# Kernel tuning notes

Hardware: AMD Instinct MI355X
Metric: run time of the kernel (lower is better)

## Reference

```python
import jax, jax.numpy as jnp
import numpy as np

TOP_K = 2


def setup_inputs() -> dict:
    key = jax.random.key(0)
    k0, k1, k2, k3, k4 = jax.random.split(key, 5)
    B, S, H, I, E = 4, 2048, 1024, 2816, 8
    s_h = 1.0 / np.sqrt(H)
    s_i = 1.0 / np.sqrt(I)
    return {
        "x": jax.random.normal(k0, (B, S, H), jnp.float32),
        # nn.Linear weights are stored as [out_features, in_features]
        "w_router": jax.random.normal(k1, (E, H), jnp.float32) * s_h,   # gate: H -> E
        "w_gate": jax.random.normal(k2, (E, I, H), jnp.float32) * s_h,  # per-expert gate_proj
        "w_up": jax.random.normal(k3, (E, I, H), jnp.float32) * s_h,    # per-expert up_proj
        "w_down": jax.random.normal(k4, (E, H, I), jnp.float32) * s_i,  # per-expert down_proj
    }


def reference(x, w_router, w_gate, w_up, w_down):
    B, S, H = x.shape
    E = w_router.shape[0]
    xf = x.reshape(-1, H)                      # [T, H], T = B*S

    # --- Router: softmax over experts, top-k, renormalize weights ---
    logits = jnp.einsum("th,eh->te", xf, w_router)        # [T, E]
    probs = jax.nn.softmax(logits, axis=-1)
    topw, topi = jax.lax.top_k(probs, TOP_K)              # [T, k]
    topw = topw / jnp.sum(topw, axis=-1, keepdims=True)

    # Per-token combine weight for each expert: sum_k w[t,k] * 1[idx[t,k]==e]
    onehot = (topi[..., None] == jnp.arange(E)).astype(x.dtype)  # [T, k, E]
    combine = jnp.einsum("tk,tke->te", topw, onehot)             # [T, E]

    # --- Experts: SwiGLU MLP per expert on all tokens, masked combine ---
    # (masked-dense in the original == gather-compute mathematically,
    # since silu(0)*0 = 0 and the projections have no bias)
    gate = jax.nn.silu(jnp.einsum("th,eih->eti", xf, w_gate))    # [E, T, I]
    up = jnp.einsum("th,eih->eti", xf, w_up)                     # [E, T, I]
    down = jnp.einsum("eti,ehi->eth", gate * up, w_down)         # [E, T, H]

    out = jnp.einsum("eth,te->th", down, combine)                # [T, H]
    return out.reshape(B, S, H)
```

## Files before the change

kernel.cpp:

```cpp
#include <hip/hip_runtime.h>

#define TT 8192
#define HD 1024
#define ID 2816
#define NE 8
#define NID2 (2*ID)

typedef __attribute__((ext_vector_type(8))) short short8;
typedef __attribute__((ext_vector_type(4))) float f32x4;

#define WS_TOP2I 0
#define WS_TOP2W 65536
#define WS_CNT   131072
#define WS_OFF   131136
#define WS_CUR   131200
#define WS_TMAP  131328
#define WS_SLOTW 196864
#define WS_T2S   262400
#define WS_XB    1048576ULL
#define WS_WGU   (WS_XB  + 16777216ULL)
#define WS_WDB   (WS_WGU + 92274688ULL)
#define WS_ACT   (WS_WDB + 46137344ULL)

__device__ __forceinline__ unsigned int pack_bf2(float lo, float hi) {
  unsigned int ul = __builtin_bit_cast(unsigned int, lo) + 0x8000u;
  unsigned int uh = __builtin_bit_cast(unsigned int, hi) + 0x8000u;
  return (uh & 0xffff0000u) | (ul >> 16);
}

__device__ __forceinline__ unsigned short f2bf(float f) {
  unsigned int u = __builtin_bit_cast(unsigned int, f);
  return (unsigned short)((u + 0x8000u) >> 16);
}

__device__ __forceinline__ void gload16(const void* g, void* l) {
  __builtin_amdgcn_global_load_lds(
      (const __attribute__((address_space(1))) unsigned int*)g,
      (__attribute__((address_space(3))) unsigned int*)l, 16, 0, 0);
}

__global__ __launch_bounds__(256) void router_kernel(
    const float* __restrict__ x, const float* __restrict__ wr,
    int* __restrict__ top2i, float* __restrict__ top2w,
    unsigned short* __restrict__ xb)
{
  int tid  = threadIdx.x;
  int lane = tid & 63;
  int t    = blockIdx.x * 4 + (tid >> 6);

  const float4* xp = (const float4*)(x + (size_t)t * HD + lane * 16);
  float4 xv[4];
  #pragma unroll
  for (int j = 0; j < 4; ++j) xv[j] = xp[j];

  uint4 v0, v1;
  v0.x = pack_bf2(xv[0].x, xv[0].y); v0.y = pack_bf2(xv[0].z, xv[0].w);
  v0.z = pack_bf2(xv[1].x, xv[1].y); v0.w = pack_bf2(xv[1].z, xv[1].w);
  v1.x = pack_bf2(xv[2].x, xv[2].y); v1.y = pack_bf2(xv[2].z, xv[2].w);
  v1.z = pack_bf2(xv[3].x, xv[3].y); v1.w = pack_bf2(xv[3].z, xv[3].w);
  uint4* xrow = (uint4*)(xb + (size_t)t * HD + lane * 16);
  xrow[0] = v0; xrow[1] = v1;

  float acc[NE];
  #pragma unroll
  for (int e = 0; e < NE; ++e) {
    const float4* wp = (const float4*)(wr + (size_t)e * HD + lane * 16);
    float s = 0.f;
    #pragma unroll
    for (int j = 0; j < 4; ++j) {
      float4 w = wp[j];
      s += xv[j].x * w.x + xv[j].y * w.y + xv[j].z * w.z + xv[j].w * w.w;
    }
    acc[e] = s;
  }
  #pragma unroll
  for (int d = 1; d < 64; d <<= 1) {
    #pragma unroll
    for (int e = 0; e < NE; ++e) acc[e] += __shfl_xor(acc[e], d, 64);
  }
  int   i0 = 0; float m0 = acc[0];
  #pragma unroll
  for (int e = 1; e < NE; ++e) if (acc[e] > m0) { m0 = acc[e]; i0 = e; }
  int   i1 = -1; float m1 = -3.4e38f;
  #pragma unroll
  for (int e = 0; e < NE; ++e) if (e != i0 && acc[e] > m1) { m1 = acc[e]; i1 = e; }

  float e1 = __expf(m1 - m0);
  float w0 = 1.f / (1.f + e1);
  float w1 = e1 * w0;

  if (lane == 0) {
    top2i[2 * t] = i0;  top2i[2 * t + 1] = i1;
    top2w[2 * t] = w0;  top2w[2 * t + 1] = w1;
  }
}

__global__ __launch_bounds__(256) void count_scan_kernel(
    const int* __restrict__ top2i,
    int* __restrict__ counts, int* __restrict__ offsets, int* __restrict__ cursors)
{
  __shared__ int s_cnt[NE];
  int tid = threadIdx.x;
  if (tid < NE) s_cnt[tid] = 0;
  __syncthreads();

  int c0=0,c1=0,c2=0,c3=0,c4=0,c5=0,c6=0,c7=0;
  for (int t = tid; t < TT; t += 256) {
    int e0 = top2i[2 * t], e1 = top2i[2 * t + 1];
    c0 += __popcll(__ballot(e0 == 0)) + __popcll(__ballot(e1 == 0));
    c1 += __popcll(__ballot(e0 == 1)) + __popcll(__ballot(e1 == 1));
    c2 += __popcll(__ballot(e0 == 2)) + __popcll(__ballot(e1 == 2));
    c3 += __popcll(__ballot(e0 == 3)) + __popcll(__ballot(e1 == 3));
    c4 += __popcll(__ballot(e0 == 4)) + __popcll(__ballot(e1 == 4));
    c5 += __popcll(__ballot(e0 == 5)) + __popcll(__ballot(e1 == 5));
    c6 += __popcll(__ballot(e0 == 6)) + __popcll(__ballot(e1 == 6));
    c7 += __popcll(__ballot(e0 == 7)) + __popcll(__ballot(e1 == 7));
  }
  if ((tid & 63) == 0) {
    atomicAdd(&s_cnt[0], c0); atomicAdd(&s_cnt[1], c1);
    atomicAdd(&s_cnt[2], c2); atomicAdd(&s_cnt[3], c3);
    atomicAdd(&s_cnt[4], c4); atomicAdd(&s_cnt[5], c5);
    atomicAdd(&s_cnt[6], c6); atomicAdd(&s_cnt[7], c7);
  }
  __syncthreads();
  if (tid == 0) {
    int run = 0;
    #pragma unroll
    for (int e = 0; e < NE; ++e) {
      counts[e] = s_cnt[e]; offsets[e] = run; cursors[e] = run; run += s_cnt[e];
    }
    offsets[NE] = run;
  }
}

__global__ __launch_bounds__(256) void place_kernel(
    const int* __restrict__ top2i, const float* __restrict__ top2w,
    int* __restrict__ cursors,
    int* __restrict__ token_map, float* __restrict__ slot_w, int* __restrict__ tok2slot)
{
  int tid  = threadIdx.x;
  int lane = tid & 63;
  int t    = blockIdx.x * 256 + tid;

  #pragma unroll
  for (int k = 0; k < 2; ++k) {
    int   e = top2i[2 * t + k];
    float w = top2w[2 * t + k];
    #pragma unroll
    for (int ee = 0; ee < NE; ++ee) {
      unsigned long long m = __ballot(e == ee);
      if (e == ee) {
        int leader = __ffsll((long long)m) - 1;
        int pre    = __popcll(m & ((1ull << lane) - 1ull));
        int base   = 0;
        if (lane == leader) base = atomicAdd(&cursors[ee], (int)__popcll(m));
        base = __shfl(base, leader, 64);
        token_map[base + pre] = t;
        slot_w[base + pre]    = w;
        tok2slot[2 * t + k]   = base + pre;
      }
    }
  }
}

__global__ __launch_bounds__(256) void cvt_wgu_kernel(
    const float* __restrict__ wg, const float* __restrict__ wu,
    unsigned short* __restrict__ wgu)
{
  int e   = blockIdx.y;
  int idx = blockIdx.x * 256 + threadIdx.x;
  int col8 = idx & 127;
  int rr   = idx >> 7;
  int blk  = rr >> 8;
  int win  = rr & 255;
  const float* srow = (win < 128)
      ? wg + ((size_t)e * ID + blk * 128 + win) * HD
      : wu + ((size_t)e * ID + blk * 128 + (win - 128)) * HD;
  const float4* p = (const float4*)(srow + col8 * 8);
  float4 a = p[0], b = p[1];
  uint4 v;
  v.x = pack_bf2(a.x, a.y); v.y = pack_bf2(a.z, a.w);
  v.z = pack_bf2(b.x, b.y); v.w = pack_bf2(b.z, b.w);
  *(uint4*)(wgu + ((size_t)e * NID2 + rr) * HD + col8 * 8) = v;
}

__global__ __launch_bounds__(256) void cvt_bf16_kernel(
    const float* __restrict__ in, unsigned short* __restrict__ out, int n8)
{
  int i = blockIdx.x * 256 + threadIdx.x;
  if (i >= n8) return;
  const float4* p = (const float4*)(in + (size_t)i * 8);
  float4 a = p[0], b = p[1];
  uint4 v;
  v.x = pack_bf2(a.x, a.y); v.y = pack_bf2(a.z, a.w);
  v.z = pack_bf2(b.x, b.y); v.w = pack_bf2(b.z, b.w);
  ((uint4*)out)[i] = v;
}


#define VW(N) asm volatile("s_waitcnt vmcnt(" #N ")" ::: "memory")
#define BAR() __builtin_amdgcn_s_barrier()

#define ISSUE(t) { \
    size_t k1 = (size_t)((t) * 32); \
    char* db = ldsc + (((t) & 3) * 32768u) + (unsigned)tid * 16; \
    gload16(aS[0] + k1, db);            gload16(aS[1] + k1, db + 8192); \
    gload16(bS[0] + k1, db + 16384);    gload16(bS[1] + k1, db + 24576); }

#define BODY(t) { \
    const char* sa = ldsc + (((t) & 3) * 32768u); \
    const char* sb = sa + 16384; \
    short8 af[8], bfr[4]; \
    _Pragma("unroll") for (int n = 0; n < 4; ++n) \
      bfr[n] = *(const short8*)(sb + (wc * 64 + n * 16 + arow) * 64 + kx); \
    _Pragma("unroll") for (int m = 0; m < 8; ++m) \
      af[m] = *(const short8*)(sa + (wr * 128 + m * 16 + arow) * 64 + kx); \
    __builtin_amdgcn_s_setprio(1); \
    _Pragma("unroll") for (int m = 0; m < 8; ++m) \
      _Pragma("unroll") for (int n = 0; n < 4; ++n) \
        acc[m][n] = __builtin_amdgcn_mfma_f32_16x16x32_bf16(af[m], bfr[n], acc[m][n], 0, 0, 0); \
    __builtin_amdgcn_s_setprio(0); }

#define KLOOP(NT) { \
    ISSUE(0); ISSUE(1); ISSUE(2); \
    int t = 0; \
    for (; t < (NT) - 3; ++t) { VW(8); BAR(); ISSUE(t + 3); BODY(t); } \
    VW(8); BAR(); BODY(t); ++t; \
    VW(4); BAR(); BODY(t); ++t; \
    VW(0); BAR(); BODY(t); }

#define XCD_DECODE(NX, NY) \
  int nwg  = (NX) * (NY) * NE; \
  int flat = blockIdx.x + (NX) * (blockIdx.y + (NY) * blockIdx.z); \
  int qq   = nwg >> 3; \
  int wg   = (flat & 7) * qq + (flat >> 3); \
  int bx   = wg % (NX); \
  int rem  = wg / (NX); \
  int y    = rem % (NY); \
  int e    = rem / (NY);

__global__ __launch_bounds__(512, 2) void gemm1_fast(
    const unsigned short* __restrict__ xb, const unsigned short* __restrict__ wgu,
    const int* __restrict__ counts, const int* __restrict__ offsets,
    const int* __restrict__ token_map, unsigned short* __restrict__ act)
{
  extern __shared__ char smem[];
  char* ldsc = smem;

  XCD_DECODE(8, 22)
  int cnt = counts[e];
  int off = offsets[e];

  int tid  = threadIdx.x;
  int lane = tid & 63;
  int w    = tid >> 6;
  int wr   = w >> 2;
  int wc   = w & 3;

  int srow = tid >> 2;
  int colE = (((tid & 3) ^ ((tid >> 2) & 3)) << 3);
  int arow = lane & 15;
  int kx   = (((lane >> 4) ^ (lane & 3)) << 4);
  int prow = (lane >> 4) << 2;

  for (int t0 = bx * 256; t0 < cnt; t0 += 2048) {
    const unsigned short* aS[2];
    const unsigned short* bS[2];
    #pragma unroll
    for (int j = 0; j < 2; ++j) {
      int row  = srow + 128 * j;
      int tr   = t0 + row;
      int slot = off + (tr < cnt ? tr : cnt - 1);
      aS[j] = xb  + (size_t)token_map[slot] * HD + colE;
      bS[j] = wgu + ((size_t)e * NID2 + (size_t)y * 256 + row) * HD + colE;
    }

    f32x4 zf = {0.f, 0.f, 0.f, 0.f};
    f32x4 acc[8][4];
    #pragma unroll
    for (int m = 0; m < 8; ++m)
      #pragma unroll
      for (int n = 0; n < 4; ++n) acc[m][n] = zf;

    KLOOP(HD / 32);

    __syncthreads();
    float* xch = (float*)smem;
    if (wc >= 2) {
      float* base = xch + (size_t)((wr * 2 + (wc - 2)) * 8192);
      #pragma unroll
      for (int m = 0; m < 8; ++m)
        #pragma unroll
        for (int n = 0; n < 4; ++n)
          #pragma unroll
          for (int r = 0; r < 4; ++r)
            base[(m * 16 + prow + r) * 64 + n * 16 + arow] = acc[m][n][r];
    }
    __syncthreads();
    if (wc < 2) {
      const float* base = xch + (size_t)((wr * 2 + wc) * 8192);
      int i0 = y * 128 + wc * 64;
      #pragma unroll
      for (int m = 0; m < 8; ++m) {
        #pragma unroll
        for (int r = 0; r < 4; ++r) {
          int row = wr * 128 + m * 16 + prow + r;
          int tr2 = t0 + row;
          if (tr2 >= cnt) continue;
          size_t ob = (size_t)(off + tr2) * ID + i0 + arow;
          #pragma unroll
          for (int n = 0; n < 4; ++n) {
            float g = acc[m][n][r];
            float u = base[(m * 16 + prow + r) * 64 + n * 16 + arow];
            float h = g * u / (1.f + __expf(-g));
            act[ob + n * 16] = f2bf(h);
          }
        }
      }
    }
    __syncthreads();
  }
}

__global__ __launch_bounds__(512, 2) void gemm2_fast(
    const unsigned short* __restrict__ act, const unsigned short* __restrict__ wdb,
    const int* __restrict__ counts, const int* __restrict__ offsets,
    float* __restrict__ down)
{
  extern __shared__ char smem[];
  char* ldsc = smem;

  XCD_DECODE(8, 4)
  int cnt = counts[e];
  int off = offsets[e];

  int tid  = threadIdx.x;
  int lane = tid & 63;
  int w    = tid >> 6;
  int wr   = w >> 2;
  int wc   = w & 3;

  int srow = tid >> 2;
  int colE = (((tid & 3) ^ ((tid >> 2) & 3)) << 3);
  int arow = lane & 15;
  int kx   = (((lane >> 4) ^ (lane & 3)) << 4);
  int prow = (lane >> 4) << 2;

  for (int t0 = bx * 256; t0 < cnt; t0 += 2048) {
    const unsigned short* aS[2];
    const unsigned short* bS[2];
    #pragma unroll
    for (int j = 0; j < 2; ++j) {
      int row  = srow + 128 * j;
      int tr   = t0 + row;
      int slot = off + (tr < cnt ? tr : cnt - 1);
      aS[j] = act + (size_t)slot * ID + colE;
      bS[j] = wdb + ((size_t)e * HD + (size_t)y * 256 + row) * ID + colE;
    }

    f32x4 zf = {0.f, 0.f, 0.f, 0.f};
    f32x4 acc[8][4];
    #pragma unroll
    for (int m = 0; m < 8; ++m)
      #pragma unroll
      for (int n = 0; n < 4; ++n) acc[m][n] = zf;

    KLOOP(ID / 32);

    #pragma unroll
    for (int m = 0; m < 8; ++m) {
      #pragma unroll
      for (int r = 0; r < 4; ++r) {
        int row = wr * 128 + m * 16 + prow + r;
        int tr2 = t0 + row;
        if (tr2 >= cnt) continue;
        float* ob = down + (size_t)(off + tr2) * HD + (size_t)y * 256 + wc * 64 + arow;
        #pragma unroll
        for (int n = 0; n < 4; ++n)
          ob[n * 16] = acc[m][n][r];
      }
    }
    __syncthreads();
  }
}

__global__ __launch_bounds__(256) void combine_kernel(
    const float* __restrict__ down, const float* __restrict__ slot_w,
    const int* __restrict__ tok2slot, float* __restrict__ out)
{
  int t   = blockIdx.x;
  int tid = threadIdx.x;
  int s0  = tok2slot[2 * t], s1 = tok2slot[2 * t + 1];
  float w0 = slot_w[s0], w1 = slot_w[s1];
  const float4* d0 = (const float4*)(down + (size_t)s0 * HD) + tid;
  const float4* d1 = (const float4*)(down + (size_t)s1 * HD) + tid;
  float4 a = *d0, b = *d1;
  float4 o;
  o.x = w0 * a.x + w1 * b.x;  o.y = w0 * a.y + w1 * b.y;
  o.z = w0 * a.z + w1 * b.z;  o.w = w0 * a.w + w1 * b.w;
  ((float4*)(out + (size_t)t * HD))[tid] = o;
}

extern "C" void kernel_launch(void* const* d_in, const int* in_sizes, int n_in,
                              void* d_out, int out_size, void* d_ws, size_t ws_size,
                              hipStream_t stream) {
  const float* x        = (const float*)d_in[0];
  const float* w_router = (const float*)d_in[1];
  const float* w_gate   = (const float*)d_in[2];
  const float* w_up     = (const float*)d_in[3];
  const float* w_down   = (const float*)d_in[4];

  char* ws = (char*)d_ws;
  int*   top2i    = (int*)(ws + WS_TOP2I);
  float* top2w    = (float*)(ws + WS_TOP2W);
  int*   counts   = (int*)(ws + WS_CNT);
  int*   offsets  = (int*)(ws + WS_OFF);
  int*   cursors  = (int*)(ws + WS_CUR);
  int*   tmap     = (int*)(ws + WS_TMAP);
  float* slotw    = (float*)(ws + WS_SLOTW);
  int*   tok2slot = (int*)(ws + WS_T2S);
  unsigned short* xb  = (unsigned short*)(ws + WS_XB);
  unsigned short* wgu = (unsigned short*)(ws + WS_WGU);
  unsigned short* wdb = (unsigned short*)(ws + WS_WDB);
  unsigned short* act = (unsigned short*)(ws + WS_ACT);
  float*          down = (float*)(ws + WS_WGU);

  hipFuncSetAttribute((const void*)gemm1_fast,
                      hipFuncAttributeMaxDynamicSharedMemorySize, 131072);
  hipFuncSetAttribute((const void*)gemm2_fast,
                      hipFuncAttributeMaxDynamicSharedMemorySize, 131072);

  router_kernel<<<TT / 4, 256, 0, stream>>>(x, w_router, top2i, top2w, xb);
  count_scan_kernel<<<1, 256, 0, stream>>>(top2i, counts, offsets, cursors);
  place_kernel<<<TT / 256, 256, 0, stream>>>(top2i, top2w, cursors, tmap, slotw, tok2slot);
  cvt_wgu_kernel<<<dim3(2816, NE), 256, 0, stream>>>(w_gate, w_up, wgu);
  cvt_bf16_kernel<<<11264, 256, 0, stream>>>(w_down, wdb, NE * HD * ID / 8);

  gemm1_fast<<<dim3(8, 22, NE), 512, 131072, stream>>>(xb, wgu, counts, offsets, tmap, act);
  gemm2_fast<<<dim3(8, 4, NE), 512, 131072, stream>>>(act, wdb, counts, offsets, down);
  combine_kernel<<<TT, 256, 0, stream>>>(down, slotw, tok2slot, (float*)d_out);
}
```

Before: 654.2 us.

## Shrink expert GEMM tiles to 128x128 with single-buffered LDS and more blocks

Both expert GEMMs drop from 256x256 tiles with 512 threads and a 4-deep async LDS ring (128 KB) to 128x128 tiles with 256 threads, one 32 KB static LDS stage of K=64, and a new XOR swizzle. The gate/up interleave in the converted weights changes from 128-row to 64-row blocks to match the smaller N tile. The aim is more workgroups and higher occupancy, which should balance load across uneven expert counts. The cost is losing the multi-stage prefetch pipeline (sync, load, sync, compute), plus lower per-tile data reuse and more global traffic.

```diff
diff --git a/kernel.cpp b/kernel.cpp
--- a/kernel.cpp
+++ b/kernel.cpp
@@ -167,15 +167,15 @@
     const float* __restrict__ wg, const float* __restrict__ wu,
     unsigned short* __restrict__ wgu)
 {
-  int e   = blockIdx.y;
-  int idx = blockIdx.x * 256 + threadIdx.x;
+  int e    = blockIdx.y;
+  int idx  = blockIdx.x * 256 + threadIdx.x;
   int col8 = idx & 127;
   int rr   = idx >> 7;
-  int blk  = rr >> 8;
-  int win  = rr & 255;
-  const float* srow = (win < 128)
-      ? wg + ((size_t)e * ID + blk * 128 + win) * HD
-      : wu + ((size_t)e * ID + blk * 128 + (win - 128)) * HD;
+  int blk  = rr >> 7;
+  int win  = rr & 127;
+  const float* srow = (win < 64)
+      ? wg + ((size_t)e * ID + blk * 64 + win) * HD
+      : wu + ((size_t)e * ID + blk * 64 + (win - 64)) * HD;
   const float4* p = (const float4*)(srow + col8 * 8);
   float4 a = p[0], b = p[1];
   uint4 v;
@@ -198,36 +198,37 @@
 }
 
 
-#define VW(N) asm volatile("s_waitcnt vmcnt(" #N ")" ::: "memory")
-#define BAR() __builtin_amdgcn_s_barrier()
-
-#define ISSUE(t) { \
-    size_t k1 = (size_t)((t) * 32); \
-    char* db = ldsc + (((t) & 3) * 32768u) + (unsigned)tid * 16; \
-    gload16(aS[0] + k1, db);            gload16(aS[1] + k1, db + 8192); \
-    gload16(bS[0] + k1, db + 16384);    gload16(bS[1] + k1, db + 24576); }
-
-#define BODY(t) { \
-    const char* sa = ldsc + (((t) & 3) * 32768u); \
-    const char* sb = sa + 16384; \
-    short8 af[8], bfr[4]; \
-    _Pragma("unroll") for (int n = 0; n < 4; ++n) \
-      bfr[n] = *(const short8*)(sb + (wc * 64 + n * 16 + arow) * 64 + kx); \
-    _Pragma("unroll") for (int m = 0; m < 8; ++m) \
-      af[m] = *(const short8*)(sa + (wr * 128 + m * 16 + arow) * 64 + kx); \
-    __builtin_amdgcn_s_setprio(1); \
-    _Pragma("unroll") for (int m = 0; m < 8; ++m) \
+#define STG(kt) { \
+    size_t k1 = (size_t)((kt) * 64); \
+    char* db = ldsc + (unsigned)tid * 16; \
+    _Pragma("unroll") for (int c = 0; c < 4; ++c) { \
+      gload16(aS[c] + k1, db + c * 4096); \
+      gload16(bS[c] + k1, db + 16384 + c * 4096); } }
+
+#define CMP() { \
+    const char* sa = ldsc; \
+    const char* sb = ldsc + 16384; \
+    _Pragma("unroll") for (int kk = 0; kk < 2; ++kk) { \
+      int kb = kk * 64 + kq; \
+      short8 af[4], bfr[4]; \
       _Pragma("unroll") for (int n = 0; n < 4; ++n) \
-        acc[m][n] = __builtin_amdgcn_mfma_f32_16x16x32_bf16(af[m], bfr[n], acc[m][n], 0, 0, 0); \
-    __builtin_amdgcn_s_setprio(0); }
+        bfr[n] = *(const short8*)(sb + (wcn * 64 + n * 16 + arow) * 128 + (kb ^ rxor)); \
+      _Pragma("unroll") for (int m = 0; m < 4; ++m) \
+        af[m] = *(const short8*)(sa + (wr * 64 + m * 16 + arow) * 128 + (kb ^ rxor)); \
+      __builtin_amdgcn_s_setprio(1); \
+      _Pragma("unroll") for (int m = 0; m < 4; ++m) \
+        _Pragma("unroll") for (int n = 0; n < 4; ++n) \
+          acc[m][n] = __builtin_amdgcn_mfma_f32_16x16x32_bf16(af[m], bfr[n], acc[m][n], 0, 0, 0); \
+      __builtin_amdgcn_s_setprio(0); \
+    } }
 
 #define KLOOP(NT) { \
-    ISSUE(0); ISSUE(1); ISSUE(2); \
-    int t = 0; \
-    for (; t < (NT) - 3; ++t) { VW(8); BAR(); ISSUE(t + 3); BODY(t); } \
-    VW(8); BAR(); BODY(t); ++t; \
-    VW(4); BAR(); BODY(t); ++t; \
-    VW(0); BAR(); BODY(t); }
+    for (int kt = 0; kt < (NT); ++kt) { \
+      if (kt) __syncthreads(); \
+      STG(kt); \
+      __syncthreads(); \
+      CMP(); \
+    } }
 
 #define XCD_DECODE(NX, NY) \
   int nwg  = (NX) * (NY) * NE; \
@@ -239,57 +240,57 @@
   int y    = rem % (NY); \
   int e    = rem / (NY);
 
-__global__ __launch_bounds__(512, 2) void gemm1_fast(
+__global__ __launch_bounds__(256, 4) void gemm1_fast(
     const unsigned short* __restrict__ xb, const unsigned short* __restrict__ wgu,
     const int* __restrict__ counts, const int* __restrict__ offsets,
     const int* __restrict__ token_map, unsigned short* __restrict__ act)
 {
-  extern __shared__ char smem[];
+  __shared__ __align__(16) char smem[32768];
   char* ldsc = smem;
 
-  XCD_DECODE(8, 22)
+  XCD_DECODE(16, 44)
   int cnt = counts[e];
   int off = offsets[e];
 
   int tid  = threadIdx.x;
   int lane = tid & 63;
   int w    = tid >> 6;
-  int wr   = w >> 2;
-  int wc   = w & 3;
-
-  int srow = tid >> 2;
-  int colE = (((tid & 3) ^ ((tid >> 2) & 3)) << 3);
+  int wr   = w >> 1;
+  int wcn  = w & 1;
+
+  int sr8  = tid >> 3;
+  int colE = (((tid & 7) ^ (sr8 & 7)) << 3);
+  int rxor = (lane & 7) << 4;
   int arow = lane & 15;
-  int kx   = (((lane >> 4) ^ (lane & 3)) << 4);
+  int kq   = (lane >> 4) << 4;
   int prow = (lane >> 4) << 2;
 
-  for (int t0 = bx * 256; t0 < cnt; t0 += 2048) {
-    const unsigned short* aS[2];
-    const unsigned short* bS[2];
-    #pragma unroll
-    for (int j = 0; j < 2; ++j) {
-      int row  = srow + 128 * j;
-      int tr   = t0 + row;
-      int slot = off + (tr < cnt ? tr : cnt - 1);
-      aS[j] = xb  + (size_t)token_map[slot] * HD + colE;
-      bS[j] = wgu + ((size_t)e * NID2 + (size_t)y * 256 + row) * HD + colE;
+  for (int t0 = bx * 128; t0 < cnt; t0 += 2048) {
+    const unsigned short* aS[4];
+    const unsigned short* bS[4];
+    #pragma unroll
+    for (int c = 0; c < 4; ++c) {
+      int rowA = t0 + c * 32 + sr8;
+      int slot = off + (rowA < cnt ? rowA : cnt - 1);
+      aS[c] = xb  + (size_t)token_map[slot] * HD + colE;
+      bS[c] = wgu + ((size_t)e * NID2 + (size_t)y * 128 + c * 32 + sr8) * HD + colE;
     }
 
     f32x4 zf = {0.f, 0.f, 0.f, 0.f};
-    f32x4 acc[8][4];
-    #pragma unroll
-    for (int m = 0; m < 8; ++m)
+    f32x4 acc[4][4];
+    #pragma unroll
+    for (int m = 0; m < 4; ++m)
       #pragma unroll
       for (int n = 0; n < 4; ++n) acc[m][n] = zf;
 
-    KLOOP(HD / 32);
+    KLOOP(HD / 64);
 
     __syncthreads();
     float* xch = (float*)smem;
-    if (wc >= 2) {
-      float* base = xch + (size_t)((wr * 2 + (wc - 2)) * 8192);
+    if (wcn == 1) {
+      float* base = xch + wr * 4096;
       #pragma unroll
-      for (int m = 0; m < 8; ++m)
+      for (int m = 0; m < 4; ++m)
         #pragma unroll
         for (int n = 0; n < 4; ++n)
           #pragma unroll
@@ -297,17 +298,16 @@
             base[(m * 16 + prow + r) * 64 + n * 16 + arow] = acc[m][n][r];
     }
     __syncthreads();
-    if (wc < 2) {
-      const float* base = xch + (size_t)((wr * 2 + wc) * 8192);
-      int i0 = y * 128 + wc * 64;
+    if (wcn == 0) {
+      const float* base = xch + wr * 4096;
       #pragma unroll
-      for (int m = 0; m < 8; ++m) {
+      for (int m = 0; m < 4; ++m) {
         #pragma unroll
         for (int r = 0; r < 4; ++r) {
-          int row = wr * 128 + m * 16 + prow + r;
+          int row = wr * 64 + m * 16 + prow + r;
           int tr2 = t0 + row;
           if (tr2 >= cnt) continue;
-          size_t ob = (size_t)(off + tr2) * ID + i0 + arow;
+          size_t ob = (size_t)(off + tr2) * ID + (size_t)y * 64 + arow;
           #pragma unroll
           for (int n = 0; n < 4; ++n) {
             float g = acc[m][n][r];
@@ -322,59 +322,59 @@
   }
 }
 
-__global__ __launch_bounds__(512, 2) void gemm2_fast(
+__global__ __launch_bounds__(256, 4) void gemm2_fast(
     const unsigned short* __restrict__ act, const unsigned short* __restrict__ wdb,
     const int* __restrict__ counts, const int* __restrict__ offsets,
     float* __restrict__ down)
 {
-  extern __shared__ char smem[];
+  __shared__ __align__(16) char smem[32768];
   char* ldsc = smem;
 
-  XCD_DECODE(8, 4)
+  XCD_DECODE(16, 8)
   int cnt = counts[e];
   int off = offsets[e];
 
   int tid  = threadIdx.x;
   int lane = tid & 63;
   int w    = tid >> 6;
-  int wr   = w >> 2;
-  int wc   = w & 3;
-
-  int srow = tid >> 2;
-  int colE = (((tid & 3) ^ ((tid >> 2) & 3)) << 3);
+  int wr   = w >> 1;
+  int wcn  = w & 1;
+
+  int sr8  = tid >> 3;
+  int colE = (((tid & 7) ^ (sr8 & 7)) << 3);
+  int rxor = (lane & 7) << 4;
   int arow = lane & 15;
-  int kx   = (((lane >> 4) ^ (lane & 3)) << 4);
+  int kq   = (lane >> 4) << 4;
   int prow = (lane >> 4) << 2;
 
-  for (int t0 = bx * 256; t0 < cnt; t0 += 2048) {
-    const unsigned short* aS[2];
-    const unsigned short* bS[2];
-    #pragma unroll
-    for (int j = 0; j < 2; ++j) {
-      int row  = srow + 128 * j;
-      int tr   = t0 + row;
-      int slot = off + (tr < cnt ? tr : cnt - 1);
-      aS[j] = act + (size_t)slot * ID + colE;
-      bS[j] = wdb + ((size_t)e * HD + (size_t)y * 256 + row) * ID + colE;
+  for (int t0 = bx * 128; t0 < cnt; t0 += 2048) {
+    const unsigned short* aS[4];
+    const unsigned short* bS[4];
+    #pragma unroll
+    for (int c = 0; c < 4; ++c) {
+      int rowA = t0 + c * 32 + sr8;
+      int slot = off + (rowA < cnt ? rowA : cnt - 1);
+      aS[c] = act + (size_t)slot * ID + colE;
+      bS[c] = wdb + ((size_t)e * HD + (size_t)y * 128 + c * 32 + sr8) * ID + colE;
     }
 
     f32x4 zf = {0.f, 0.f, 0.f, 0.f};
-    f32x4 acc[8][4];
-    #pragma unroll
-    for (int m = 0; m < 8; ++m)
+    f32x4 acc[4][4];
+    #pragma unroll
+    for (int m = 0; m < 4; ++m)
       #pragma unroll
       for (int n = 0; n < 4; ++n) acc[m][n] = zf;
 
-    KLOOP(ID / 32);
-
-    #pragma unroll
-    for (int m = 0; m < 8; ++m) {
+    KLOOP(ID / 64);
+
+    #pragma unroll
+    for (int m = 0; m < 4; ++m) {
       #pragma unroll
       for (int r = 0; r < 4; ++r) {
-        int row = wr * 128 + m * 16 + prow + r;
+        int row = wr * 64 + m * 16 + prow + r;
         int tr2 = t0 + row;
         if (tr2 >= cnt) continue;
-        float* ob = down + (size_t)(off + tr2) * HD + (size_t)y * 256 + wc * 64 + arow;
+        float* ob = down + (size_t)(off + tr2) * HD + (size_t)y * 128 + wcn * 64 + arow;
         #pragma unroll
         for (int n = 0; n < 4; ++n)
           ob[n * 16] = acc[m][n][r];
@@ -425,18 +425,13 @@
   unsigned short* act = (unsigned short*)(ws + WS_ACT);
   float*          down = (float*)(ws + WS_WGU);
 
-  hipFuncSetAttribute((const void*)gemm1_fast,
-                      hipFuncAttributeMaxDynamicSharedMemorySize, 131072);
-  hipFuncSetAttribute((const void*)gemm2_fast,
-                      hipFuncAttributeMaxDynamicSharedMemorySize, 131072);
-
   router_kernel<<<TT / 4, 256, 0, stream>>>(x, w_router, top2i, top2w, xb);
   count_scan_kernel<<<1, 256, 0, stream>>>(top2i, counts, offsets, cursors);
   place_kernel<<<TT / 256, 256, 0, stream>>>(top2i, top2w, cursors, tmap, slotw, tok2slot);
   cvt_wgu_kernel<<<dim3(2816, NE), 256, 0, stream>>>(w_gate, w_up, wgu);
   cvt_bf16_kernel<<<11264, 256, 0, stream>>>(w_down, wdb, NE * HD * ID / 8);
 
-  gemm1_fast<<<dim3(8, 22, NE), 512, 131072, stream>>>(xb, wgu, counts, offsets, tmap, act);
-  gemm2_fast<<<dim3(8, 4, NE), 512, 131072, stream>>>(act, wdb, counts, offsets, down);
+  gemm1_fast<<<dim3(16, 44, NE), 256, 0, stream>>>(xb, wgu, counts, offsets, tmap, act);
+  gemm2_fast<<<dim3(16, 8, NE), 256, 0, stream>>>(act, wdb, counts, offsets, down);
   combine_kernel<<<TT, 256, 0, stream>>>(down, slotw, tok2slot, (float*)d_out);
 }
```

Result: no change. 652.7 us (-0.2%).
